# Performance work log

Measured on AMD Instinct MI355X. Metric: run time of the kernel, lower is better.

## Reference

```python
import jax, jax.numpy as jnp
import numpy as np

CURV = 0.01
EPS = 1e-15


def _artanh(x):
    x = jnp.clip(x, -1.0 + 1e-7, 1.0 - 1e-7)
    return 0.5 * jnp.log((1.0 + x) / (1.0 - x))


def log_map_zero(x, c):
    sqrt_c = jnp.sqrt(c)
    norm = jnp.maximum(jnp.linalg.norm(x, axis=-1, keepdims=True), EPS)
    return _artanh(sqrt_c * norm) * x / (sqrt_c * norm)


def exp_map_zero(v, c):
    sqrt_c = jnp.sqrt(c)
    norm = jnp.maximum(jnp.linalg.norm(v, axis=-1, keepdims=True), EPS)
    return jnp.tanh(sqrt_c * norm) * v / (sqrt_c * norm)


def mobius_add(x, y, c):
    # Works with broadcasting over leading dims.
    x2 = jnp.sum(x * x, axis=-1, keepdims=True)
    y2 = jnp.sum(y * y, axis=-1, keepdims=True)
    xy = jnp.sum(x * y, axis=-1, keepdims=True)
    num = (1.0 + 2.0 * c * xy + c * y2) * x + (1.0 - c * x2) * y
    den = 1.0 + 2.0 * c * xy + (c * c) * x2 * y2
    return num / jnp.maximum(den, EPS)


def givens_rotation(x, angles):
    # x: (B, d), angles: (d/2,)
    B, d = x.shape
    x1, x2 = x[:, 0::2], x[:, 1::2]
    ca, sa = jnp.cos(angles)[None, :], jnp.sin(angles)[None, :]
    out1 = ca * x1 - sa * x2
    out2 = sa * x1 + ca * x2
    return jnp.stack([out1, out2], axis=2).reshape(B, d)


def givens_reflection(x, angles):
    B, d = x.shape
    x1, x2 = x[:, 0::2], x[:, 1::2]
    ca, sa = jnp.cos(angles)[None, :], jnp.sin(angles)[None, :]
    out1 = ca * x1 + sa * x2
    out2 = sa * x1 - ca * x2
    return jnp.stack([out1, out2], axis=2).reshape(B, d)


def setup_inputs() -> dict:
    key = jax.random.key(0)
    ks = jax.random.split(key, 8)
    num_entities, num_rels, d, B = 20000, 250, 256, 2048
    R = num_rels * 2
    PI = float(np.pi)
    entity_embedding = 0.1 * jax.random.normal(ks[0], (num_entities, d), dtype=jnp.float32)
    rel_embedding = jax.random.normal(ks[1], (R, d), dtype=jnp.float32)
    s = jax.random.randint(ks[2], (B,), 0, num_entities)
    r = jax.random.randint(ks[3], (B,), 0, R)
    o = jax.random.randint(ks[4], (B,), 0, num_entities)
    triplets = jnp.stack([s, r, o], axis=1).astype(jnp.int64)
    global_rot = jax.random.uniform(ks[5], (d // 2,), minval=-PI, maxval=PI, dtype=jnp.float32)
    global_ref = jax.random.uniform(ks[6], (d // 2,), minval=-PI, maxval=PI, dtype=jnp.float32)
    attn_weight = 0.01 * jax.random.normal(ks[7], (2 * d,), dtype=jnp.float32)
    rel_bias = jnp.zeros((R,), dtype=jnp.float32)
    return {
        "entity_embedding": entity_embedding,
        "rel_embedding": rel_embedding,
        "triplets": triplets,
        "global_rot": global_rot,
        "global_ref": global_ref,
        "attn_weight": attn_weight,
        "rel_bias": rel_bias,
    }


def reference(entity_embedding, rel_embedding, triplets, global_rot, global_ref, attn_weight, rel_bias):
    c = CURV
    s_emb = entity_embedding[triplets[:, 0]]        # (B, d)
    o_emb = entity_embedding[triplets[:, 2]]        # (B, d)
    s_tan = log_map_zero(s_emb, c)
    o_tan = log_map_zero(o_emb, c)
    # dropout p=0 -> identity
    rot_s = givens_rotation(s_tan, global_rot)
    ref_s = givens_reflection(s_tan, global_ref)
    attn_input = jnp.concatenate([s_tan, o_tan], axis=-1)   # (B, 2d)
    a = jax.nn.sigmoid(attn_input @ attn_weight)[:, None]   # (B, 1)
    mixed_tan = a * rot_s + (1.0 - a) * ref_s
    mixed_hyp = exp_map_zero(mixed_tan, c)
    query = mobius_add(-mixed_hyp, o_emb, c)                # (B, d)
    rel_hyp = exp_map_zero(rel_embedding, c)                # (R, d)
    # broadcast Mobius distance: (B, 1, d) vs (1, R, d)
    diff = mobius_add(-query[:, None, :], rel_hyp[None, :, :], c)
    dist_sq = jnp.sum(diff * diff, axis=-1)                 # (B, R)
    scores = -dist_sq + rel_bias[None, :]
    return scores
```

## Files before the change

kernel.cpp:

```cpp
#include <hip/hip_runtime.h>
#include <hip/hip_bf16.h>
#include <math.h>

#define D 256
#define BATCH 2048
#define NREL 500
#define NRELP 512
#define CURV_C 0.01f
#define SQRT_C 0.1f

typedef __attribute__((ext_vector_type(8))) short s16x8;
typedef __attribute__((ext_vector_type(4))) float f32x4;

__device__ __forceinline__ float wave_reduce(float v) {
    #pragma unroll
    for (int off = 1; off < 64; off <<= 1) v += __shfl_xor(v, off, 64);
    return v;
}

__device__ __forceinline__ float dot4(float4 a, float4 b) {
    return a.x * b.x + a.y * b.y + a.z * b.z + a.w * b.w;
}

__device__ __forceinline__ float tanh_fast(float x) {
    float e = __expf(2.0f * x);
    return 1.0f - 2.0f / (e + 1.0f);
}
__device__ __forceinline__ float artanh_fast(float z) {
    z = fminf(fmaxf(z, -1.0f + 1e-7f), 1.0f - 1e-7f);
    return 0.5f * __logf((1.0f + z) / (1.0f - z));
}

__device__ __forceinline__ unsigned short f2bf(float x) {
    union { float f; unsigned int u; } c; c.f = x;
    unsigned int r = (c.u + 0x7fffu + ((c.u >> 16) & 1u)) >> 16;
    return (unsigned short)r;
}
__device__ __forceinline__ float bf2f(unsigned short h) {
    union { unsigned int u; float f; } c; c.u = ((unsigned int)h) << 16;
    return c.f;
}

__device__ __forceinline__ void store_hilo(unsigned short* ph, unsigned short* pl, float4 v) {
    ushort4 h, lo;
    #pragma unroll
    for (int e = 0; e < 4; ++e) {
        float x = (&v.x)[e];
        unsigned short hb = f2bf(x);
        float hf = bf2f(hb);
        (&h.x)[e] = hb;
        (&lo.x)[e] = f2bf(x - hf);
    }
    *(ushort4*)ph = h;
    *(ushort4*)pl = lo;
}

__global__ __launch_bounds__(256) void prep_kernel(
    const float* __restrict__ ent, const float* __restrict__ rel,
    const int* __restrict__ trip,
    const float* __restrict__ grot, const float* __restrict__ gref,
    const float* __restrict__ attw,
    unsigned short* __restrict__ Qh, unsigned short* __restrict__ Ql,
    float* __restrict__ q2out,
    unsigned short* __restrict__ Hh, unsigned short* __restrict__ Hl,
    float* __restrict__ r2out)
{
    const int w = blockIdx.x * 4 + (threadIdx.x >> 6);
    const int l = threadIdx.x & 63;

    if (w < NRELP) {
        const int r = w;
        float4 v = make_float4(0.f, 0.f, 0.f, 0.f);
        if (r < NREL) v = *(const float4*)&rel[(size_t)r * D + 4 * l];
        float n2 = wave_reduce(dot4(v, v));
        float n = fmaxf(sqrtf(n2), 1e-15f);
        float f = tanh_fast(SQRT_C * n) / (SQRT_C * n);
        float4 hv = make_float4(f * v.x, f * v.y, f * v.z, f * v.w);
        store_hilo(&Hh[(size_t)r * D + 4 * l], &Hl[(size_t)r * D + 4 * l], hv);
        if (l == 0) r2out[r] = f * f * n2;
    } else if (w < NRELP + BATCH) {
        const int b = w - NRELP;
        const int s = trip[3 * b + 0];
        const int o = trip[3 * b + 2];
        float4 se = *(const float4*)&ent[(size_t)s * D + 4 * l];
        float4 oe = *(const float4*)&ent[(size_t)o * D + 4 * l];

        float ns2 = wave_reduce(dot4(se, se));
        float no2 = wave_reduce(dot4(oe, oe));
        float ns = fmaxf(sqrtf(ns2), 1e-15f);
        float no = fmaxf(sqrtf(no2), 1e-15f);
        float fs = artanh_fast(SQRT_C * ns) / (SQRT_C * ns);
        float fo = artanh_fast(SQRT_C * no) / (SQRT_C * no);
        float4 st = make_float4(fs * se.x, fs * se.y, fs * se.z, fs * se.w);
        float4 ot = make_float4(fo * oe.x, fo * oe.y, fo * oe.z, fo * oe.w);

        float4 wa = *(const float4*)&attw[4 * l];
        float4 wb = *(const float4*)&attw[D + 4 * l];
        float adot = wave_reduce(dot4(st, wa) + dot4(ot, wb));
        float a = 1.0f / (1.0f + __expf(-adot));

        float2 ar = ((const float2*)grot)[l];
        float2 af = ((const float2*)gref)[l];
        float ca0 = __cosf(ar.x), sa0 = __sinf(ar.x);
        float ca1 = __cosf(ar.y), sa1 = __sinf(ar.y);
        float cr0 = __cosf(af.x), sr0 = __sinf(af.x);
        float cr1 = __cosf(af.y), sr1 = __sinf(af.y);

        float4 rot = make_float4(ca0 * st.x - sa0 * st.y, sa0 * st.x + ca0 * st.y,
                                 ca1 * st.z - sa1 * st.w, sa1 * st.z + ca1 * st.w);
        float4 rfl = make_float4(cr0 * st.x + sr0 * st.y, sr0 * st.x - cr0 * st.y,
                                 cr1 * st.z + sr1 * st.w, sr1 * st.z - cr1 * st.w);
        float ia = 1.0f - a;
        float4 mt = make_float4(a * rot.x + ia * rfl.x, a * rot.y + ia * rfl.y,
                                a * rot.z + ia * rfl.z, a * rot.w + ia * rfl.w);

        float nm2 = wave_reduce(dot4(mt, mt));
        float nm = fmaxf(sqrtf(nm2), 1e-15f);
        float fm = tanh_fast(SQRT_C * nm) / (SQRT_C * nm);
        float4 mh = make_float4(fm * mt.x, fm * mt.y, fm * mt.z, fm * mt.w);
        float x2v = fm * fm * nm2;

        float xy = wave_reduce(-dot4(mh, oe));
        const float c = CURV_C;
        float A  = 1.0f + 2.0f * c * xy + c * no2;
        float Bf = 1.0f - c * x2v;
        float den = fmaxf(1.0f + 2.0f * c * xy + c * c * x2v * no2, 1e-15f);
        float inv = 1.0f / den;
        float4 q = make_float4((A * -mh.x + Bf * oe.x) * inv,
                               (A * -mh.y + Bf * oe.y) * inv,
                               (A * -mh.z + Bf * oe.z) * inv,
                               (A * -mh.w + Bf * oe.w) * inv);
        store_hilo(&Qh[(size_t)b * D + 4 * l], &Ql[(size_t)b * D + 4 * l], q);
        if (l == 0) {
            float num2 = A * A * x2v + 2.0f * A * Bf * xy + Bf * Bf * no2;
            q2out[b] = num2 * inv * inv;
        }
    }
}

__global__ __launch_bounds__(512) void score_kernel(
    const unsigned short* __restrict__ Qh, const unsigned short* __restrict__ Ql,
    const float* __restrict__ q2,
    const unsigned short* __restrict__ Hh, const unsigned short* __restrict__ Hl,
    const float* __restrict__ r2,
    const float* __restrict__ bias, float* __restrict__ out)
{
    __shared__ __align__(16) unsigned char lds[131072];
    const int t = threadIdx.x;
    const int m0 = blockIdx.x * 64, n0 = blockIdx.y * 64;
    const int w = t >> 6;
    const int l = t & 63;

    {
        const int rsub = l >> 5;
        const int cl = l & 31;
        #pragma unroll
        for (int it = 0; it < 4; ++it) {
            const int r = w * 8 + it * 2 + rsub;
            const unsigned int csw = (unsigned int)((cl ^ (r & 7)) * 8);
            const unsigned int loff = (unsigned int)(w * 4096 + it * 1024);
            const size_t gA = (size_t)(m0 + r) * D + csw;
            const size_t gB = (size_t)(n0 + r) * D + csw;
            __builtin_amdgcn_global_load_lds(
                (const __attribute__((address_space(1))) void*)(Qh + gA),
                (__attribute__((address_space(3))) void*)(lds + loff), 16, 0, 0);
            __builtin_amdgcn_global_load_lds(
                (const __attribute__((address_space(1))) void*)(Ql + gA),
                (__attribute__((address_space(3))) void*)(lds + 32768 + loff), 16, 0, 0);
            __builtin_amdgcn_global_load_lds(
                (const __attribute__((address_space(1))) void*)(Hh + gB),
                (__attribute__((address_space(3))) void*)(lds + 65536 + loff), 16, 0, 0);
            __builtin_amdgcn_global_load_lds(
                (const __attribute__((address_space(1))) void*)(Hl + gB),
                (__attribute__((address_space(3))) void*)(lds + 98304 + loff), 16, 0, 0);
        }
    }
    __syncthreads();

    const int wm = w >> 2;
    const int wn = w & 3;
    const int lr = l & 15;
    const int lk = l >> 4;
    const unsigned int sw = (unsigned int)((lr & 7) << 4);

    f32x4 acc[2];
    acc[0] = (f32x4){0.f, 0.f, 0.f, 0.f};
    acc[1] = (f32x4){0.f, 0.f, 0.f, 0.f};

    const unsigned int bbase = (unsigned int)((wn * 16 + lr) * 512);
    const unsigned int abase = (unsigned int)((wm * 32 + lr) * 512);
    #pragma unroll
    for (int ks = 0; ks < 8; ++ks) {
        const unsigned int coff = ((unsigned int)(ks * 4 + lk) << 4) ^ sw;
        s16x8 bh = *(const s16x8*)(lds + 65536 + bbase + coff);
        s16x8 bl = *(const s16x8*)(lds + 98304 + bbase + coff);
        #pragma unroll
        for (int mi = 0; mi < 2; ++mi) {
            const unsigned int aoff = abase + (unsigned int)(mi * 16 * 512) + coff;
            s16x8 ah = *(const s16x8*)(lds + aoff);
            s16x8 al = *(const s16x8*)(lds + 32768 + aoff);
            acc[mi] = __builtin_amdgcn_mfma_f32_16x16x32_bf16(ah, bh, acc[mi], 0, 0, 0);
            acc[mi] = __builtin_amdgcn_mfma_f32_16x16x32_bf16(ah, bl, acc[mi], 0, 0, 0);
            acc[mi] = __builtin_amdgcn_mfma_f32_16x16x32_bf16(al, bh, acc[mi], 0, 0, 0);
        }
    }

    const int n = n0 + wn * 16 + lr;
    const bool nok = (n < NREL);
    float y2v = 0.f, biasv = 0.f;
    if (nok) { y2v = r2[n]; biasv = bias[n]; }
    const float c = CURV_C;
    #pragma unroll
    for (int mi = 0; mi < 2; ++mi) {
        #pragma unroll
        for (int rg = 0; rg < 4; ++rg) {
            const int m = m0 + wm * 32 + mi * 16 + lk * 4 + rg;
            const float x2 = q2[m];
            const float Bf = 1.0f - c * x2;
            const float xy = -acc[mi][rg];
            const float A  = 1.0f + 2.0f * c * xy + c * y2v;
            const float den = fmaxf(1.0f + 2.0f * c * xy + c * c * x2 * y2v, 1e-15f);
            const float num2 = A * A * x2 + 2.0f * A * Bf * xy + Bf * Bf * y2v;
            if (nok) out[(size_t)m * NREL + n] = biasv - num2 / (den * den);
        }
    }
}

extern "C" void kernel_launch(void* const* d_in, const int* in_sizes, int n_in,
                              void* d_out, int out_size, void* d_ws, size_t ws_size,
                              hipStream_t stream) {
    const float* ent  = (const float*)d_in[0];
    const float* rel  = (const float*)d_in[1];
    const int*   trip = (const int*)d_in[2];
    const float* grot = (const float*)d_in[3];
    const float* gref = (const float*)d_in[4];
    const float* attw = (const float*)d_in[5];
    const float* bias = (const float*)d_in[6];
    float* out = (float*)d_out;

    char* ws = (char*)d_ws;
    unsigned short* Qh = (unsigned short*)(ws);
    unsigned short* Ql = (unsigned short*)(ws + (1u << 20));
    unsigned short* Hh = (unsigned short*)(ws + (2u << 20));
    unsigned short* Hl = (unsigned short*)(ws + (2u << 20) + (256u << 10));
    float* q2 = (float*)(ws + (2u << 20) + (512u << 10));
    float* r2 = (float*)(ws + (2u << 20) + (512u << 10) + 8192);

    const int nwaves = NRELP + BATCH;
    prep_kernel<<<nwaves / 4, 256, 0, stream>>>(ent, rel, trip, grot, gref, attw,
                                                Qh, Ql, q2, Hh, Hl, r2);
    dim3 grid(BATCH / 64, NRELP / 64);
    score_kernel<<<grid, 512, 0, stream>>>(Qh, Ql, q2, Hh, Hl, r2, bias, out);
}
```

Baseline: 15.64 us.

## Fuse prep and score kernels, recomputing query and relation tiles per block

```diff
diff --git a/kernel.cpp b/kernel.cpp
--- a/kernel.cpp
+++ b/kernel.cpp
@@ -5,21 +5,36 @@
 #define D 256
 #define BATCH 2048
 #define NREL 500
-#define NRELP 512
 #define CURV_C 0.01f
 #define SQRT_C 0.1f
 
 typedef __attribute__((ext_vector_type(8))) short s16x8;
 typedef __attribute__((ext_vector_type(4))) float f32x4;
 
-__device__ __forceinline__ float wave_reduce(float v) {
-    #pragma unroll
-    for (int off = 1; off < 64; off <<= 1) v += __shfl_xor(v, off, 64);
-    return v;
-}
-
 __device__ __forceinline__ float dot4(float4 a, float4 b) {
     return a.x * b.x + a.y * b.y + a.z * b.z + a.w * b.w;
+}
+
+__device__ __forceinline__ float wave_reduce1(float a) {
+    #pragma unroll
+    for (int off = 1; off < 64; off <<= 1) a += __shfl_xor(a, off, 64);
+    return a;
+}
+__device__ __forceinline__ void wave_reduce2(float& a, float& b) {
+    #pragma unroll
+    for (int off = 1; off < 64; off <<= 1) {
+        a += __shfl_xor(a, off, 64);
+        b += __shfl_xor(b, off, 64);
+    }
+}
+__device__ __forceinline__ void wave_reduce4(float& a, float& b, float& c, float& d) {
+    #pragma unroll
+    for (int off = 1; off < 64; off <<= 1) {
+        a += __shfl_xor(a, off, 64);
+        b += __shfl_xor(b, off, 64);
+        c += __shfl_xor(c, off, 64);
+        d += __shfl_xor(d, off, 64);
+    }
 }
 
 __device__ __forceinline__ float tanh_fast(float x) {
@@ -40,163 +55,141 @@
     union { unsigned int u; float f; } c; c.u = ((unsigned int)h) << 16;
     return c.f;
 }
-
-__device__ __forceinline__ void store_hilo(unsigned short* ph, unsigned short* pl, float4 v) {
-    ushort4 h, lo;
+__device__ __forceinline__ void pack_hilo(float4 v, ushort4& h, ushort4& lo) {
     #pragma unroll
     for (int e = 0; e < 4; ++e) {
         float x = (&v.x)[e];
         unsigned short hb = f2bf(x);
-        float hf = bf2f(hb);
         (&h.x)[e] = hb;
-        (&lo.x)[e] = f2bf(x - hf);
-    }
-    *(ushort4*)ph = h;
-    *(ushort4*)pl = lo;
-}
-
-__global__ __launch_bounds__(256) void prep_kernel(
+        (&lo.x)[e] = f2bf(x - bf2f(hb));
+    }
+}
+
+__global__ __launch_bounds__(512, 2) void fused_kernel(
     const float* __restrict__ ent, const float* __restrict__ rel,
     const int* __restrict__ trip,
     const float* __restrict__ grot, const float* __restrict__ gref,
-    const float* __restrict__ attw,
-    unsigned short* __restrict__ Qh, unsigned short* __restrict__ Ql,
-    float* __restrict__ q2out,
-    unsigned short* __restrict__ Hh, unsigned short* __restrict__ Hl,
-    float* __restrict__ r2out)
+    const float* __restrict__ attw, const float* __restrict__ bias,
+    float* __restrict__ out)
 {
-    const int w = blockIdx.x * 4 + (threadIdx.x >> 6);
-    const int l = threadIdx.x & 63;
-
-    if (w < NRELP) {
-        const int r = w;
-        float4 v = make_float4(0.f, 0.f, 0.f, 0.f);
-        if (r < NREL) v = *(const float4*)&rel[(size_t)r * D + 4 * l];
-        float n2 = wave_reduce(dot4(v, v));
-        float n = fmaxf(sqrtf(n2), 1e-15f);
-        float f = tanh_fast(SQRT_C * n) / (SQRT_C * n);
-        float4 hv = make_float4(f * v.x, f * v.y, f * v.z, f * v.w);
-        store_hilo(&Hh[(size_t)r * D + 4 * l], &Hl[(size_t)r * D + 4 * l], hv);
-        if (l == 0) r2out[r] = f * f * n2;
-    } else if (w < NRELP + BATCH) {
-        const int b = w - NRELP;
+    __shared__ __align__(16) unsigned char lds[131072];
+    __shared__ float q2s[64];
+    __shared__ float r2s[64];
+
+    const int t = threadIdx.x;
+    const int bx = blockIdx.x;
+    const int w = t >> 6, l = t & 63;
+    const int m0 = (bx & 31) * 64;
+    const int n0 = (bx >> 5) * 64;
+
+    const float4 wa = *(const float4*)&attw[4 * l];
+    const float4 wb = *(const float4*)&attw[D + 4 * l];
+    const float2 ar = ((const float2*)grot)[l];
+    const float2 af = ((const float2*)gref)[l];
+    const float ca0 = __cosf(ar.x), sa0 = __sinf(ar.x);
+    const float ca1 = __cosf(ar.y), sa1 = __sinf(ar.y);
+    const float cr0 = __cosf(af.x), sr0 = __sinf(af.x);
+    const float cr1 = __cosf(af.y), sr1 = __sinf(af.y);
+
+    const unsigned ch = (unsigned)(l >> 1);
+    const unsigned sub8 = (unsigned)((l & 1) * 8);
+
+    float4 se8[8], oe8[8];
+    #pragma unroll
+    for (int i = 0; i < 8; ++i) {
+        const int b = m0 + w * 8 + i;
         const int s = trip[3 * b + 0];
         const int o = trip[3 * b + 2];
-        float4 se = *(const float4*)&ent[(size_t)s * D + 4 * l];
-        float4 oe = *(const float4*)&ent[(size_t)o * D + 4 * l];
-
-        float ns2 = wave_reduce(dot4(se, se));
-        float no2 = wave_reduce(dot4(oe, oe));
-        float ns = fmaxf(sqrtf(ns2), 1e-15f);
-        float no = fmaxf(sqrtf(no2), 1e-15f);
-        float fs = artanh_fast(SQRT_C * ns) / (SQRT_C * ns);
-        float fo = artanh_fast(SQRT_C * no) / (SQRT_C * no);
-        float4 st = make_float4(fs * se.x, fs * se.y, fs * se.z, fs * se.w);
-        float4 ot = make_float4(fo * oe.x, fo * oe.y, fo * oe.z, fo * oe.w);
-
-        float4 wa = *(const float4*)&attw[4 * l];
-        float4 wb = *(const float4*)&attw[D + 4 * l];
-        float adot = wave_reduce(dot4(st, wa) + dot4(ot, wb));
-        float a = 1.0f / (1.0f + __expf(-adot));
-
-        float2 ar = ((const float2*)grot)[l];
-        float2 af = ((const float2*)gref)[l];
-        float ca0 = __cosf(ar.x), sa0 = __sinf(ar.x);
-        float ca1 = __cosf(ar.y), sa1 = __sinf(ar.y);
-        float cr0 = __cosf(af.x), sr0 = __sinf(af.x);
-        float cr1 = __cosf(af.y), sr1 = __sinf(af.y);
-
-        float4 rot = make_float4(ca0 * st.x - sa0 * st.y, sa0 * st.x + ca0 * st.y,
-                                 ca1 * st.z - sa1 * st.w, sa1 * st.z + ca1 * st.w);
-        float4 rfl = make_float4(cr0 * st.x + sr0 * st.y, sr0 * st.x - cr0 * st.y,
-                                 cr1 * st.z + sr1 * st.w, sr1 * st.z - cr1 * st.w);
-        float ia = 1.0f - a;
-        float4 mt = make_float4(a * rot.x + ia * rfl.x, a * rot.y + ia * rfl.y,
-                                a * rot.z + ia * rfl.z, a * rot.w + ia * rfl.w);
-
-        float nm2 = wave_reduce(dot4(mt, mt));
-        float nm = fmaxf(sqrtf(nm2), 1e-15f);
-        float fm = tanh_fast(SQRT_C * nm) / (SQRT_C * nm);
-        float4 mh = make_float4(fm * mt.x, fm * mt.y, fm * mt.z, fm * mt.w);
-        float x2v = fm * fm * nm2;
-
-        float xy = wave_reduce(-dot4(mh, oe));
+        se8[i] = *(const float4*)&ent[(size_t)s * D + 4 * l];
+        oe8[i] = *(const float4*)&ent[(size_t)o * D + 4 * l];
+    }
+
+    #pragma unroll
+    for (int i = 0; i < 8; ++i) {
+        const int r = w * 8 + i;
+        const int gn = n0 + r;
+        float4 v = make_float4(0.f, 0.f, 0.f, 0.f);
+        if (gn < NREL) v = *(const float4*)&rel[(size_t)gn * D + 4 * l];
+        float n2 = wave_reduce1(dot4(v, v));
+        float nn = fmaxf(sqrtf(n2), 1e-15f);
+        float f = tanh_fast(SQRT_C * nn) / (SQRT_C * nn);
+        float4 hv = make_float4(f * v.x, f * v.y, f * v.z, f * v.w);
+        ushort4 h, lo; pack_hilo(hv, h, lo);
+        const unsigned off = (unsigned)(r * 512) + ((ch ^ (unsigned)(r & 7)) << 4) + sub8;
+        *(ushort4*)(lds + 65536 + off) = h;
+        *(ushort4*)(lds + 98304 + off) = lo;
+        if (l == 0) r2s[r] = f * f * n2;
+    }
+
+    #pragma unroll
+    for (int i = 0; i < 8; ++i) {
+        const int r = w * 8 + i;
+        const float4 se = se8[i], oe = oe8[i];
+        float ns2 = dot4(se, se), no2 = dot4(oe, oe);
+        float dsw = dot4(se, wa), dow = dot4(oe, wb);
+        wave_reduce4(ns2, no2, dsw, dow);
+        const float ns = fmaxf(sqrtf(ns2), 1e-15f);
+        const float no = fmaxf(sqrtf(no2), 1e-15f);
+        const float fs = artanh_fast(SQRT_C * ns) / (SQRT_C * ns);
+        const float fo = artanh_fast(SQRT_C * no) / (SQRT_C * no);
+        const float adot = fs * dsw + fo * dow;
+        const float a = 1.0f / (1.0f + __expf(-adot));
+        const float4 st = make_float4(fs * se.x, fs * se.y, fs * se.z, fs * se.w);
+        const float4 rot = make_float4(ca0 * st.x - sa0 * st.y, sa0 * st.x + ca0 * st.y,
+                                       ca1 * st.z - sa1 * st.w, sa1 * st.z + ca1 * st.w);
+        const float4 rfl = make_float4(cr0 * st.x + sr0 * st.y, sr0 * st.x - cr0 * st.y,
+                                       cr1 * st.z + sr1 * st.w, sr1 * st.z - cr1 * st.w);
+        const float ia = 1.0f - a;
+        const float4 mt = make_float4(a * rot.x + ia * rfl.x, a * rot.y + ia * rfl.y,
+                                      a * rot.z + ia * rfl.z, a * rot.w + ia * rfl.w);
+        float nm2 = dot4(mt, mt), mtoe = dot4(mt, oe);
+        wave_reduce2(nm2, mtoe);
+        const float nm = fmaxf(sqrtf(nm2), 1e-15f);
+        const float fm = tanh_fast(SQRT_C * nm) / (SQRT_C * nm);
+        const float x2v = fm * fm * nm2;
+        const float xy = -fm * mtoe;
         const float c = CURV_C;
-        float A  = 1.0f + 2.0f * c * xy + c * no2;
-        float Bf = 1.0f - c * x2v;
-        float den = fmaxf(1.0f + 2.0f * c * xy + c * c * x2v * no2, 1e-15f);
-        float inv = 1.0f / den;
-        float4 q = make_float4((A * -mh.x + Bf * oe.x) * inv,
-                               (A * -mh.y + Bf * oe.y) * inv,
-                               (A * -mh.z + Bf * oe.z) * inv,
-                               (A * -mh.w + Bf * oe.w) * inv);
-        store_hilo(&Qh[(size_t)b * D + 4 * l], &Ql[(size_t)b * D + 4 * l], q);
+        const float A  = 1.0f + 2.0f * c * xy + c * no2;
+        const float Bf = 1.0f - c * x2v;
+        const float den = fmaxf(1.0f + 2.0f * c * xy + c * c * x2v * no2, 1e-15f);
+        const float inv = 1.0f / den;
+        const float Afm = A * fm;
+        const float4 q = make_float4((Bf * oe.x - Afm * mt.x) * inv,
+                                     (Bf * oe.y - Afm * mt.y) * inv,
+                                     (Bf * oe.z - Afm * mt.z) * inv,
+                                     (Bf * oe.w - Afm * mt.w) * inv);
+        ushort4 h, lo; pack_hilo(q, h, lo);
+        const unsigned off = (unsigned)(r * 512) + ((ch ^ (unsigned)(r & 7)) << 4) + sub8;
+        *(ushort4*)(lds + off) = h;
+        *(ushort4*)(lds + 32768 + off) = lo;
         if (l == 0) {
-            float num2 = A * A * x2v + 2.0f * A * Bf * xy + Bf * Bf * no2;
-            q2out[b] = num2 * inv * inv;
+            const float num2 = A * A * x2v + 2.0f * A * Bf * xy + Bf * Bf * no2;
+            q2s[r] = num2 * inv * inv;
         }
     }
-}
-
-__global__ __launch_bounds__(512) void score_kernel(
-    const unsigned short* __restrict__ Qh, const unsigned short* __restrict__ Ql,
-    const float* __restrict__ q2,
-    const unsigned short* __restrict__ Hh, const unsigned short* __restrict__ Hl,
-    const float* __restrict__ r2,
-    const float* __restrict__ bias, float* __restrict__ out)
-{
-    __shared__ __align__(16) unsigned char lds[131072];
-    const int t = threadIdx.x;
-    const int m0 = blockIdx.x * 64, n0 = blockIdx.y * 64;
-    const int w = t >> 6;
-    const int l = t & 63;
-
-    {
-        const int rsub = l >> 5;
-        const int cl = l & 31;
-        #pragma unroll
-        for (int it = 0; it < 4; ++it) {
-            const int r = w * 8 + it * 2 + rsub;
-            const unsigned int csw = (unsigned int)((cl ^ (r & 7)) * 8);
-            const unsigned int loff = (unsigned int)(w * 4096 + it * 1024);
-            const size_t gA = (size_t)(m0 + r) * D + csw;
-            const size_t gB = (size_t)(n0 + r) * D + csw;
-            __builtin_amdgcn_global_load_lds(
-                (const __attribute__((address_space(1))) void*)(Qh + gA),
-                (__attribute__((address_space(3))) void*)(lds + loff), 16, 0, 0);
-            __builtin_amdgcn_global_load_lds(
-                (const __attribute__((address_space(1))) void*)(Ql + gA),
-                (__attribute__((address_space(3))) void*)(lds + 32768 + loff), 16, 0, 0);
-            __builtin_amdgcn_global_load_lds(
-                (const __attribute__((address_space(1))) void*)(Hh + gB),
-                (__attribute__((address_space(3))) void*)(lds + 65536 + loff), 16, 0, 0);
-            __builtin_amdgcn_global_load_lds(
-                (const __attribute__((address_space(1))) void*)(Hl + gB),
-                (__attribute__((address_space(3))) void*)(lds + 98304 + loff), 16, 0, 0);
-        }
-    }
+
     __syncthreads();
 
     const int wm = w >> 2;
     const int wn = w & 3;
     const int lr = l & 15;
     const int lk = l >> 4;
-    const unsigned int sw = (unsigned int)((lr & 7) << 4);
+    const unsigned sw = (unsigned)((lr & 7) << 4);
 
     f32x4 acc[2];
     acc[0] = (f32x4){0.f, 0.f, 0.f, 0.f};
     acc[1] = (f32x4){0.f, 0.f, 0.f, 0.f};
 
-    const unsigned int bbase = (unsigned int)((wn * 16 + lr) * 512);
-    const unsigned int abase = (unsigned int)((wm * 32 + lr) * 512);
+    const unsigned bbase = (unsigned)((wn * 16 + lr) * 512);
+    const unsigned abase = (unsigned)((wm * 32 + lr) * 512);
     #pragma unroll
     for (int ks = 0; ks < 8; ++ks) {
-        const unsigned int coff = ((unsigned int)(ks * 4 + lk) << 4) ^ sw;
+        const unsigned coff = ((unsigned)(ks * 4 + lk) << 4) ^ sw;
         s16x8 bh = *(const s16x8*)(lds + 65536 + bbase + coff);
         s16x8 bl = *(const s16x8*)(lds + 98304 + bbase + coff);
         #pragma unroll
         for (int mi = 0; mi < 2; ++mi) {
-            const unsigned int aoff = abase + (unsigned int)(mi * 16 * 512) + coff;
+            const unsigned aoff = abase + (unsigned)(mi * 16 * 512) + coff;
             s16x8 ah = *(const s16x8*)(lds + aoff);
             s16x8 al = *(const s16x8*)(lds + 32768 + aoff);
             acc[mi] = __builtin_amdgcn_mfma_f32_16x16x32_bf16(ah, bh, acc[mi], 0, 0, 0);
@@ -205,17 +198,19 @@
         }
     }
 
-    const int n = n0 + wn * 16 + lr;
+    const int nl = wn * 16 + lr;
+    const int n = n0 + nl;
     const bool nok = (n < NREL);
-    float y2v = 0.f, biasv = 0.f;
-    if (nok) { y2v = r2[n]; biasv = bias[n]; }
+    float y2v = r2s[nl];
+    float biasv = nok ? bias[n] : 0.f;
     const float c = CURV_C;
     #pragma unroll
     for (int mi = 0; mi < 2; ++mi) {
         #pragma unroll
         for (int rg = 0; rg < 4; ++rg) {
-            const int m = m0 + wm * 32 + mi * 16 + lk * 4 + rg;
-            const float x2 = q2[m];
+            const int ml = wm * 32 + mi * 16 + lk * 4 + rg;
+            const int m = m0 + ml;
+            const float x2 = q2s[ml];
             const float Bf = 1.0f - c * x2;
             const float xy = -acc[mi][rg];
             const float A  = 1.0f + 2.0f * c * xy + c * y2v;
@@ -238,17 +233,5 @@
     const float* bias = (const float*)d_in[6];
     float* out = (float*)d_out;
 
-    char* ws = (char*)d_ws;
-    unsigned short* Qh = (unsigned short*)(ws);
-    unsigned short* Ql = (unsigned short*)(ws + (1u << 20));
-    unsigned short* Hh = (unsigned short*)(ws + (2u << 20));
-    unsigned short* Hl = (unsigned short*)(ws + (2u << 20) + (256u << 10));
-    float* q2 = (float*)(ws + (2u << 20) + (512u << 10));
-    float* r2 = (float*)(ws + (2u << 20) + (512u << 10) + 8192);
-
-    const int nwaves = NRELP + BATCH;
-    prep_kernel<<<nwaves / 4, 256, 0, stream>>>(ent, rel, trip, grot, gref, attw,
-                                                Qh, Ql, q2, Hh, Hl, r2);
-    dim3 grid(BATCH / 64, NRELP / 64);
-    score_kernel<<<grid, 512, 0, stream>>>(Qh, Ql, q2, Hh, Hl, r2, bias, out);
-}
+    fused_kernel<<<256, 512, 0, stream>>>(ent, rel, trip, grot, gref, attw, bias, out);
+}
```

After: 28.11 us. +79.7%, slower.
